# Kernel optimization log

Hardware: AMD Instinct MI355X
Metric: run time of the kernel (lower is better)

Reference implementation:

```python
import jax, jax.numpy as jnp
import numpy as np

EPS = 1e-8
HALF_BIN = 0.1 / 2.0  # discretization_param / 2


def setup_inputs() -> dict:
    key = jax.random.key(0)
    k1, k2, k3, k4, k5, k6 = jax.random.split(key, 6)
    B, K = 4194304, 3
    predicted_purchase_prob = jax.random.uniform(k1, (B,), jnp.float32, 0.01, 0.99)
    mu = jax.random.normal(k2, (K, B), jnp.float32) * 5.0 + 10.0
    sigma = jax.random.uniform(k3, (K, B), jnp.float32, 0.1, 2.0)
    weight = jax.random.uniform(k4, (K, B), jnp.float32, 0.0, 1.0)
    paid = jax.random.uniform(k5, (B,)) > 0.5
    vals = jax.random.uniform(k6, (B,), jnp.float32, 0.1, 50.0)
    true_values = jnp.where(paid, vals, 0.0)
    return {
        "predicted_purchase_prob": predicted_purchase_prob,
        "mu": mu,
        "sigma": sigma,
        "weight": weight,
        "true_values": true_values,
    }


def reference(predicted_purchase_prob, mu, sigma, weight, true_values):
    p = predicted_purchase_prob  # [B]
    targets = (true_values > 0).astype(p.dtype)  # [B]
    # BCE with torch-style log clamping at -100
    log_p = jnp.clip(jnp.log(p + 0.0), -100.0)
    log_1mp = jnp.clip(jnp.log(1.0 - p), -100.0)
    purchase_loss = -jnp.mean(targets * log_p + (1.0 - targets) * log_1mp)

    # Mixture-of-logistics discretized likelihood, vectorized over [K, B]
    inv_s = 1.0 / (sigma + EPS)  # [K, B]
    tv = true_values[None, :]  # [1, B]
    cdf_upper = jax.nn.sigmoid((tv + HALF_BIN - mu) * inv_s)
    cdf_lower = jax.nn.sigmoid((tv - HALF_BIN - mu) * inv_s)
    prob_density = jnp.maximum(cdf_upper - cdf_lower, EPS)  # clamp(min=1e-8)
    likelihood = jnp.sum(weight * prob_density, axis=0)  # [B]
    log_likelihood = jnp.log(likelihood + EPS)  # [B]

    paid_mask = true_values > 0
    n_paid = jnp.sum(paid_mask.astype(p.dtype))
    ll_sum = jnp.sum(jnp.where(paid_mask, log_likelihood, 0.0))
    ltv_loss = -jnp.where(n_paid > 0, ll_sum / jnp.maximum(n_paid, 1.0), 0.0)

    return purchase_loss + ltv_loss
```

## Files before the change

### kernel.cpp

```cpp
#include <hip/hip_runtime.h>
#include <math.h>

#define EPS 1e-8f
#define HALF_BIN 0.05f

__device__ __forceinline__ float fast_sigmoid(float x) {
    return __fdividef(1.0f, 1.0f + __expf(-x));
}

template <int K>
__global__ __launch_bounds__(256) void zimol_main(
    const float* __restrict__ p,
    const float* __restrict__ mu,
    const float* __restrict__ sigma,
    const float* __restrict__ weight,
    const float* __restrict__ tv,
    float* __restrict__ part_bce,
    float* __restrict__ part_ll,
    float* __restrict__ part_n,
    int B)
{
    const int tid    = blockIdx.x * blockDim.x + threadIdx.x;
    const int stride = gridDim.x * blockDim.x;
    const int B4 = B >> 2;

    const float4* __restrict__ p4  = (const float4*)p;
    const float4* __restrict__ tv4 = (const float4*)tv;

    float bce = 0.0f, ll = 0.0f, npaid = 0.0f;

    for (int i = tid; i < B4; i += stride) {
        float4 pf = p4[i];
        float4 tf = tv4[i];
        float pv[4] = {pf.x, pf.y, pf.z, pf.w};
        float t [4] = {tf.x, tf.y, tf.z, tf.w};
        float lik[4] = {0.0f, 0.0f, 0.0f, 0.0f};

        #pragma unroll
        for (int k = 0; k < K; ++k) {
            const size_t off = (size_t)k * (size_t)B;
            float4 mf = ((const float4*)(mu     + off))[i];
            float4 sf = ((const float4*)(sigma  + off))[i];
            float4 wf = ((const float4*)(weight + off))[i];
            float m[4] = {mf.x, mf.y, mf.z, mf.w};
            float s[4] = {sf.x, sf.y, sf.z, sf.w};
            float w[4] = {wf.x, wf.y, wf.z, wf.w};
            #pragma unroll
            for (int j = 0; j < 4; ++j) {
                float inv_s = __fdividef(1.0f, s[j] + EPS);
                float cu = fast_sigmoid((t[j] + HALF_BIN - m[j]) * inv_s);
                float cl = fast_sigmoid((t[j] - HALF_BIN - m[j]) * inv_s);
                float pd = fmaxf(cu - cl, EPS);
                lik[j] = fmaf(w[j], pd, lik[j]);
            }
        }

        #pragma unroll
        for (int j = 0; j < 4; ++j) {
            float target  = (t[j] > 0.0f) ? 1.0f : 0.0f;
            float log_p   = fmaxf(__logf(pv[j]),        -100.0f);
            float log_1mp = fmaxf(__logf(1.0f - pv[j]), -100.0f);
            bce -= target * log_p + (1.0f - target) * log_1mp;
            if (t[j] > 0.0f) {
                ll    += __logf(lik[j] + EPS);
                npaid += 1.0f;
            }
        }
    }

    if (tid == 0) {
        for (int i = B4 << 2; i < B; ++i) {
            float t = tv[i];
            float lik0 = 0.0f;
            #pragma unroll
            for (int k = 0; k < K; ++k) {
                const size_t off = (size_t)k * (size_t)B + i;
                float inv_s = __fdividef(1.0f, sigma[off] + EPS);
                float cu = fast_sigmoid((t + HALF_BIN - mu[off]) * inv_s);
                float cl = fast_sigmoid((t - HALF_BIN - mu[off]) * inv_s);
                lik0 = fmaf(weight[off], fmaxf(cu - cl, EPS), lik0);
            }
            float target  = (t > 0.0f) ? 1.0f : 0.0f;
            float log_p   = fmaxf(__logf(p[i]),        -100.0f);
            float log_1mp = fmaxf(__logf(1.0f - p[i]), -100.0f);
            bce -= target * log_p + (1.0f - target) * log_1mp;
            if (t > 0.0f) { ll += __logf(lik0 + EPS); npaid += 1.0f; }
        }
    }

    #pragma unroll
    for (int off = 32; off > 0; off >>= 1) {
        bce   += __shfl_down(bce,   off, 64);
        ll    += __shfl_down(ll,    off, 64);
        npaid += __shfl_down(npaid, off, 64);
    }

    __shared__ float sdata[3][4];
    const int wave = threadIdx.x >> 6;
    const int lane = threadIdx.x & 63;
    if (lane == 0) {
        sdata[0][wave] = bce;
        sdata[1][wave] = ll;
        sdata[2][wave] = npaid;
    }
    __syncthreads();
    if (threadIdx.x == 0) {
        float b = 0.0f, l = 0.0f, n = 0.0f;
        #pragma unroll
        for (int w = 0; w < 4; ++w) {
            b += sdata[0][w];
            l += sdata[1][w];
            n += sdata[2][w];
        }
        part_bce[blockIdx.x] = b;
        part_ll [blockIdx.x] = l;
        part_n  [blockIdx.x] = n;
    }
}

__global__ __launch_bounds__(256) void zimol_reduce(
    const float* __restrict__ part_bce,
    const float* __restrict__ part_ll,
    const float* __restrict__ part_n,
    float* __restrict__ out, int nblocks, int B)
{
    double b = 0.0, l = 0.0, n = 0.0;
    for (int i = threadIdx.x; i < nblocks; i += 256) {
        b += (double)part_bce[i];
        l += (double)part_ll[i];
        n += (double)part_n[i];
    }
    #pragma unroll
    for (int off = 32; off > 0; off >>= 1) {
        b += __shfl_down(b, off, 64);
        l += __shfl_down(l, off, 64);
        n += __shfl_down(n, off, 64);
    }
    __shared__ double sdata[3][4];
    const int wave = threadIdx.x >> 6;
    const int lane = threadIdx.x & 63;
    if (lane == 0) {
        sdata[0][wave] = b;
        sdata[1][wave] = l;
        sdata[2][wave] = n;
    }
    __syncthreads();
    if (threadIdx.x == 0) {
        double tb = 0.0, tl = 0.0, tn = 0.0;
        #pragma unroll
        for (int w = 0; w < 4; ++w) {
            tb += sdata[0][w];
            tl += sdata[1][w];
            tn += sdata[2][w];
        }
        double purchase = tb / (double)B;
        double ltv = (tn > 0.0) ? -(tl / fmax(tn, 1.0)) : 0.0;
        out[0] = (float)(purchase + ltv);
    }
}

extern "C" void kernel_launch(void* const* d_in, const int* in_sizes, int n_in,
                              void* d_out, int out_size, void* d_ws, size_t ws_size,
                              hipStream_t stream) {
    const float* p      = (const float*)d_in[0];
    const float* mu     = (const float*)d_in[1];
    const float* sigma  = (const float*)d_in[2];
    const float* weight = (const float*)d_in[3];
    const float* tv     = (const float*)d_in[4];
    float* out = (float*)d_out;

    const int B = in_sizes[0];
    const int K = in_sizes[1] / B;

    const int threads = 256;
    int blocks = ((B >> 2) + threads - 1) / threads;
    if (blocks < 1) blocks = 1;
    if (blocks > 65536) blocks = 65536;

    float* part_bce = (float*)d_ws;
    float* part_ll  = part_bce + blocks;
    float* part_n   = part_ll  + blocks;

    if (K == 3) {
        zimol_main<3><<<blocks, threads, 0, stream>>>(p, mu, sigma, weight, tv,
                                                      part_bce, part_ll, part_n, B);
    } else if (K == 1) {
        zimol_main<1><<<blocks, threads, 0, stream>>>(p, mu, sigma, weight, tv,
                                                      part_bce, part_ll, part_n, B);
    } else if (K == 2) {
        zimol_main<2><<<blocks, threads, 0, stream>>>(p, mu, sigma, weight, tv,
                                                      part_bce, part_ll, part_n, B);
    } else {
        zimol_main<4><<<blocks, threads, 0, stream>>>(p, mu, sigma, weight, tv,
                                                      part_bce, part_ll, part_n, B);
    }

    zimol_reduce<<<1, threads, 0, stream>>>(part_bce, part_ll, part_n, out, blocks, B);
}
```

Baseline: 195.7 us.

## Cap grid, unroll grid-stride loop by two, and fuse sigmoid difference

Caps the grid at 1024 blocks so each thread runs a grid-stride loop, and unrolls that loop by two so loads for two float4 groups are issued before any compute, giving more memory-level parallelism. It also merges the two sigmoids into one expression that needs a single division, and makes the BCE path branch-free with one log instead of two. Fewer blocks shrink the partial-sum reduction, at the risk of lower occupancy and of extra register pressure from the doubled loads.

```diff
diff --git a/kernel.cpp b/kernel.cpp
--- a/kernel.cpp
+++ b/kernel.cpp
@@ -4,8 +4,71 @@
 #define EPS 1e-8f
 #define HALF_BIN 0.05f
 
-__device__ __forceinline__ float fast_sigmoid(float x) {
-    return __fdividef(1.0f, 1.0f + __expf(-x));
+__device__ __forceinline__ float sigmoid_diff(float xu, float xl) {
+    float eu = __expf(fminf(-xu, 87.0f));
+    float el = __expf(fminf(-xl, 87.0f));
+    float num = el - eu;
+    float den = (1.0f + eu) * (1.0f + el);
+    return __fdividef(num, den);
+}
+
+template <int K>
+__device__ __forceinline__ void process_group(
+    const float4& pf, const float4& tf,
+    const float4 (&mf)[K], const float4 (&sf)[K], const float4 (&wf)[K],
+    float& bce, float& ll, float& npaid)
+{
+    float pv[4] = {pf.x, pf.y, pf.z, pf.w};
+    float t [4] = {tf.x, tf.y, tf.z, tf.w};
+    float lik[4] = {0.0f, 0.0f, 0.0f, 0.0f};
+
+    #pragma unroll
+    for (int k = 0; k < K; ++k) {
+        float m[4] = {mf[k].x, mf[k].y, mf[k].z, mf[k].w};
+        float s[4] = {sf[k].x, sf[k].y, sf[k].z, sf[k].w};
+        float w[4] = {wf[k].x, wf[k].y, wf[k].z, wf[k].w};
+        #pragma unroll
+        for (int j = 0; j < 4; ++j) {
+            float inv_s = __fdividef(1.0f, s[j] + EPS);
+            float xu = (t[j] + HALF_BIN - m[j]) * inv_s;
+            float xl = (t[j] - HALF_BIN - m[j]) * inv_s;
+            float pd = fmaxf(sigmoid_diff(xu, xl), EPS);
+            lik[j] = fmaf(w[j], pd, lik[j]);
+        }
+    }
+
+    #pragma unroll
+    for (int j = 0; j < 4; ++j) {
+        bool paid = t[j] > 0.0f;
+        float val = paid ? pv[j] : (1.0f - pv[j]);
+        bce -= fmaxf(__logf(val), -100.0f);
+        float lg = __logf(lik[j] + EPS);
+        ll    += paid ? lg : 0.0f;
+        npaid += paid ? 1.0f : 0.0f;
+    }
+}
+
+template <int K>
+__device__ __forceinline__ void process_elem(
+    float pv, float t, const float* mu, const float* sigma, const float* weight,
+    size_t i, size_t B, float& bce, float& ll, float& npaid)
+{
+    float lik = 0.0f;
+    #pragma unroll
+    for (int k = 0; k < K; ++k) {
+        size_t off = (size_t)k * B + i;
+        float inv_s = __fdividef(1.0f, sigma[off] + EPS);
+        float xu = (t + HALF_BIN - mu[off]) * inv_s;
+        float xl = (t - HALF_BIN - mu[off]) * inv_s;
+        float pd = fmaxf(sigmoid_diff(xu, xl), EPS);
+        lik = fmaf(weight[off], pd, lik);
+    }
+    bool paid = t > 0.0f;
+    float val = paid ? pv : (1.0f - pv);
+    bce -= fmaxf(__logf(val), -100.0f);
+    float lg = __logf(lik + EPS);
+    ll    += paid ? lg : 0.0f;
+    npaid += paid ? 1.0f : 0.0f;
 }
 
 template <int K>
@@ -22,69 +85,50 @@
 {
     const int tid    = blockIdx.x * blockDim.x + threadIdx.x;
     const int stride = gridDim.x * blockDim.x;
-    const int B4 = B >> 2;
-
-    const float4* __restrict__ p4  = (const float4*)p;
-    const float4* __restrict__ tv4 = (const float4*)tv;
 
     float bce = 0.0f, ll = 0.0f, npaid = 0.0f;
 
-    for (int i = tid; i < B4; i += stride) {
-        float4 pf = p4[i];
-        float4 tf = tv4[i];
-        float pv[4] = {pf.x, pf.y, pf.z, pf.w};
-        float t [4] = {tf.x, tf.y, tf.z, tf.w};
-        float lik[4] = {0.0f, 0.0f, 0.0f, 0.0f};
-
-        #pragma unroll
-        for (int k = 0; k < K; ++k) {
-            const size_t off = (size_t)k * (size_t)B;
-            float4 mf = ((const float4*)(mu     + off))[i];
-            float4 sf = ((const float4*)(sigma  + off))[i];
-            float4 wf = ((const float4*)(weight + off))[i];
-            float m[4] = {mf.x, mf.y, mf.z, mf.w};
-            float s[4] = {sf.x, sf.y, sf.z, sf.w};
-            float w[4] = {wf.x, wf.y, wf.z, wf.w};
-            #pragma unroll
-            for (int j = 0; j < 4; ++j) {
-                float inv_s = __fdividef(1.0f, s[j] + EPS);
-                float cu = fast_sigmoid((t[j] + HALF_BIN - m[j]) * inv_s);
-                float cl = fast_sigmoid((t[j] - HALF_BIN - m[j]) * inv_s);
-                float pd = fmaxf(cu - cl, EPS);
-                lik[j] = fmaf(w[j], pd, lik[j]);
-            }
-        }
-
-        #pragma unroll
-        for (int j = 0; j < 4; ++j) {
-            float target  = (t[j] > 0.0f) ? 1.0f : 0.0f;
-            float log_p   = fmaxf(__logf(pv[j]),        -100.0f);
-            float log_1mp = fmaxf(__logf(1.0f - pv[j]), -100.0f);
-            bce -= target * log_p + (1.0f - target) * log_1mp;
-            if (t[j] > 0.0f) {
-                ll    += __logf(lik[j] + EPS);
-                npaid += 1.0f;
-            }
-        }
-    }
-
-    if (tid == 0) {
-        for (int i = B4 << 2; i < B; ++i) {
-            float t = tv[i];
-            float lik0 = 0.0f;
+    if ((B & 3) == 0) {
+        const int B4 = B >> 2;
+        const float4* __restrict__ p4  = (const float4*)p;
+        const float4* __restrict__ tv4 = (const float4*)tv;
+        const float4* __restrict__ mu4 = (const float4*)mu;
+        const float4* __restrict__ sg4 = (const float4*)sigma;
+        const float4* __restrict__ wt4 = (const float4*)weight;
+
+        int i = tid;
+        for (; i + stride < B4; i += 2 * stride) {
+            const int i0 = i, i1 = i + stride;
+            float4 pf0  = p4[i0],  pf1  = p4[i1];
+            float4 tf0  = tv4[i0], tf1  = tv4[i1];
+            float4 mf0[K], sf0[K], wf0[K];
+            float4 mf1[K], sf1[K], wf1[K];
             #pragma unroll
             for (int k = 0; k < K; ++k) {
-                const size_t off = (size_t)k * (size_t)B + i;
-                float inv_s = __fdividef(1.0f, sigma[off] + EPS);
-                float cu = fast_sigmoid((t + HALF_BIN - mu[off]) * inv_s);
-                float cl = fast_sigmoid((t - HALF_BIN - mu[off]) * inv_s);
-                lik0 = fmaf(weight[off], fmaxf(cu - cl, EPS), lik0);
+                const size_t off = (size_t)k * (size_t)B4;
+                mf0[k] = mu4[off + i0];  mf1[k] = mu4[off + i1];
+                sf0[k] = sg4[off + i0];  sf1[k] = sg4[off + i1];
+                wf0[k] = wt4[off + i0];  wf1[k] = wt4[off + i1];
             }
-            float target  = (t > 0.0f) ? 1.0f : 0.0f;
-            float log_p   = fmaxf(__logf(p[i]),        -100.0f);
-            float log_1mp = fmaxf(__logf(1.0f - p[i]), -100.0f);
-            bce -= target * log_p + (1.0f - target) * log_1mp;
-            if (t > 0.0f) { ll += __logf(lik0 + EPS); npaid += 1.0f; }
+            process_group<K>(pf0, tf0, mf0, sf0, wf0, bce, ll, npaid);
+            process_group<K>(pf1, tf1, mf1, sf1, wf1, bce, ll, npaid);
+        }
+        for (; i < B4; i += stride) {
+            float4 pf = p4[i], tf = tv4[i];
+            float4 mf[K], sf[K], wf[K];
+            #pragma unroll
+            for (int k = 0; k < K; ++k) {
+                const size_t off = (size_t)k * (size_t)B4;
+                mf[k] = mu4[off + i];
+                sf[k] = sg4[off + i];
+                wf[k] = wt4[off + i];
+            }
+            process_group<K>(pf, tf, mf, sf, wf, bce, ll, npaid);
+        }
+    } else {
+        for (int i = tid; i < B; i += stride) {
+            process_elem<K>(p[i], tv[i], mu, sigma, weight,
+                            (size_t)i, (size_t)B, bce, ll, npaid);
         }
     }
 
@@ -173,9 +217,10 @@
     const int K = in_sizes[1] / B;
 
     const int threads = 256;
-    int blocks = ((B >> 2) + threads - 1) / threads;
+    int work = ((B + 3) >> 2);
+    int blocks = (work + threads - 1) / threads;
+    if (blocks > 1024) blocks = 1024;
     if (blocks < 1) blocks = 1;
-    if (blocks > 65536) blocks = 65536;
 
     float* part_bce = (float*)d_ws;
     float* part_ll  = part_bce + blocks;
```

Result: no change. 193.8 us (-1.0%).
